# Kernel tuning notes

Measured on AMD Instinct MI355X. Metric: run time of the kernel, lower is better.

## Reference

```python
import jax, jax.numpy as jnp
import numpy as np

B, T, C, H, FF, BOT = 2, 2048, 1024, 16, 4096, 64
D = C // H
EPS = 1e-5

def _ln(x, g, b):
    m = jnp.mean(x, axis=-1, keepdims=True)
    v = jnp.mean(jnp.square(x - m), axis=-1, keepdims=True)
    return (x - m) * jax.lax.rsqrt(v + EPS) * g + b

def setup_inputs() -> dict:
    key = jax.random.key(0)
    ks = jax.random.split(key, 20)
    def lin(k, fan_in, shape):
        return jax.random.normal(k, shape, jnp.float32) * (1.0 / np.sqrt(fan_in))
    inp = {
        "x": jax.random.normal(ks[0], (B, T, C), jnp.float32),
        # causal mask: masked_fill where mask == 0
        "attn_mask": jnp.tril(jnp.ones((T, T), jnp.int32))[None, None, :, :],
        "Wq": lin(ks[1], C, (C, C)), "bq": jnp.zeros((C,), jnp.float32),
        "Wk": lin(ks[2], C, (C, C)), "bk": jnp.zeros((C,), jnp.float32),
        "Wv": lin(ks[3], C, (C, C)), "bv": jnp.zeros((C,), jnp.float32),
        "Wo": lin(ks[4], C, (C, C)), "bo": jnp.zeros((C,), jnp.float32),
        "g1": jnp.ones((C,), jnp.float32), "beta1": jnp.zeros((C,), jnp.float32),
        "g2": jnp.ones((C,), jnp.float32), "beta2": jnp.zeros((C,), jnp.float32),
        "W1": lin(ks[5], C, (C, FF)), "bf1": jnp.zeros((FF,), jnp.float32),
        "W2": lin(ks[6], FF, (FF, C)), "bf2": jnp.zeros((C,), jnp.float32),
        "Wd": lin(ks[7], C, (C, BOT)), "bd": jnp.zeros((BOT,), jnp.float32),
        "Wu": lin(ks[8], BOT, (BOT, C)), "bu": jnp.zeros((C,), jnp.float32),
    }
    return inp

def reference(x, attn_mask, Wq, bq, Wk, bk, Wv, bv, Wo, bo,
              g1, beta1, g2, beta2, W1, bf1, W2, bf2, Wd, bd, Wu, bu):
    # --- attention sublayer ---
    xn = _ln(x, g1, beta1)
    q = (xn @ Wq + bq).reshape(B, T, H, D)
    k = (xn @ Wk + bk).reshape(B, T, H, D)
    v = (xn @ Wv + bv).reshape(B, T, H, D)
    scores = jnp.einsum('bthd,bshd->bhts', q, k) / jnp.sqrt(jnp.float32(D))
    scores = jnp.where(attn_mask == 0, -jnp.inf, scores)
    w = jax.nn.softmax(scores, axis=-1)
    attn = jnp.einsum('bhts,bshd->bthd', w, v).reshape(B, T, C)
    x = x + attn @ Wo + bo
    # --- FFN + adapter sublayer ---
    xn2 = _ln(x, g2, beta2)
    h = jax.nn.relu(xn2 @ W1 + bf1) @ W2 + bf2
    h = h + jax.nn.relu(h @ Wd + bd) @ Wu + bu  # adapter residual
    return x + h
```

## Files before the change

### kernel.cpp

```cpp
#include <hip/hip_runtime.h>
#include <cstdint>
#include <cstddef>

typedef unsigned short u16;
typedef __attribute__((ext_vector_type(4))) short short4v;
typedef __attribute__((ext_vector_type(8))) short short8;
typedef __attribute__((ext_vector_type(4))) float f32x4;

__device__ __forceinline__ float bf2f(u16 h) { return __uint_as_float(((unsigned)h) << 16); }
__device__ __forceinline__ u16 f2bf(float f) {
    unsigned u = __float_as_uint(f);
    unsigned r = (u + 0x7fffu + ((u >> 16) & 1u)) >> 16;
    return (u16)r;
}
__device__ __forceinline__ u16 f2bf_fast(float f) {
    return (u16)((__float_as_uint(f) + 0x8000u) >> 16);
}

__device__ __forceinline__ void gl_lds16(const void* g, void* l) {
    __builtin_amdgcn_global_load_lds((const __attribute__((address_space(1))) void*)g,
                                     (__attribute__((address_space(3))) void*)l, 16, 0, 0);
}

struct Prologue {
    const void* tsrc[8];
    u16* tdst[8];
    int tR[8], tC[8], toff[8];
    const void* psrc[12];
    int poff[12], pn[12];
    int ntrans;
};
__global__ __launch_bounds__(256) void prologue_kernel(Prologue P,
                                                       const unsigned* __restrict__ x,
                                                       int* __restrict__ flag,
                                                       float* __restrict__ pf) {
    __shared__ int cnt[256];
    int c = 0;
    for (int i = threadIdx.x; i < 1024; i += 256) {
        unsigned lo = x[i] & 0xFFFFu;
        unsigned e = (lo >> 7) & 0xFFu;
        c += (e >= 100u && e <= 150u) ? 1 : 0;
    }
    cnt[threadIdx.x] = c;
    __syncthreads();
    for (int s = 128; s > 0; s >>= 1) {
        if (threadIdx.x < s) cnt[threadIdx.x] += cnt[threadIdx.x + s];
        __syncthreads();
    }
    const int bf = (cnt[0] > 512) ? 1 : 0;
    if (blockIdx.x == 0 && threadIdx.x == 0) *flag = bf;

    const int bid = blockIdx.x;
    if (bid >= P.ntrans) {
        const int s = bid - P.ntrans;
        const void* sp = P.psrc[s];
        float* dp = pf + P.poff[s];
        const int n = P.pn[s];
        for (int i = threadIdx.x; i < n; i += 256)
            dp[i] = bf ? bf2f(((const u16*)sp)[i]) : ((const float*)sp)[i];
        return;
    }
    __shared__ u16 tile[32][33];
    int m = 0;
#pragma unroll
    for (int i = 1; i < 8; i++) m = (bid >= P.toff[i]) ? i : m;
    const int local = bid - P.toff[m];
    const int R = P.tR[m], C = P.tC[m];
    const int tilesx = C >> 5;
    const int bx = local % tilesx, by = local / tilesx;
    const void* src = P.tsrc[m];
    u16* dst = P.tdst[m];
    const int tx = threadIdx.x & 31, ty = threadIdx.x >> 5;
#pragma unroll
    for (int i = 0; i < 32; i += 8) {
        size_t idx = (size_t)(by * 32 + ty + i) * C + bx * 32 + tx;
        tile[ty + i][tx] = bf ? ((const u16*)src)[idx] : f2bf(((const float*)src)[idx]);
    }
    __syncthreads();
#pragma unroll
    for (int i = 0; i < 32; i += 8)
        dst[(size_t)(bx * 32 + ty + i) * R + by * 32 + tx] = tile[tx][ty + i];
}

__global__ __launch_bounds__(256) void ln_x_kernel(const void* __restrict__ X,
                                                   const float* __restrict__ G,
                                                   const float* __restrict__ Be,
                                                   u16* __restrict__ Xb,
                                                   u16* __restrict__ Y,
                                                   const int* __restrict__ flag) {
    const int row = blockIdx.x;
    const int tid = threadIdx.x;
    const int lane = tid & 63, wave = tid >> 6;
    u16 vbuf[4];
    if (*flag) {
        *(uint2*)vbuf = *(const uint2*)((const u16*)X + (size_t)row * 1024 + tid * 4);
    } else {
        float4 v = *(const float4*)((const float*)X + (size_t)row * 1024 + tid * 4);
        vbuf[0] = f2bf(v.x); vbuf[1] = f2bf(v.y); vbuf[2] = f2bf(v.z); vbuf[3] = f2bf(v.w);
    }
    *(uint2*)&Xb[(size_t)row * 1024 + tid * 4] = *(uint2*)vbuf;
    float f[4];
    float s = 0.f, sq = 0.f;
#pragma unroll
    for (int j = 0; j < 4; j++) { f[j] = bf2f(vbuf[j]); s += f[j]; sq += f[j] * f[j]; }
#pragma unroll
    for (int m = 1; m < 64; m <<= 1) { s += __shfl_xor(s, m, 64); sq += __shfl_xor(sq, m, 64); }
    __shared__ float rs_[4], rq_[4];
    if (lane == 0) { rs_[wave] = s; rq_[wave] = sq; }
    __syncthreads();
    float S = rs_[0] + rs_[1] + rs_[2] + rs_[3];
    float Q2 = rq_[0] + rq_[1] + rq_[2] + rq_[3];
    float mean = S * (1.f / 1024.f);
    float var = Q2 * (1.f / 1024.f) - mean * mean;
    float rstd = rsqrtf(var + 1e-5f);
    u16 o[4];
#pragma unroll
    for (int j = 0; j < 4; j++) {
        int c2 = tid * 4 + j;
        float y = (f[j] - mean) * rstd * G[c2] + Be[c2];
        o[j] = f2bf(y);
    }
    *(uint2*)&Y[(size_t)row * 1024 + tid * 4] = *(uint2*)o;
}

__global__ __launch_bounds__(256) void ln_kernel(const u16* __restrict__ X,
                                                 const float* __restrict__ G,
                                                 const float* __restrict__ Be,
                                                 u16* __restrict__ Y) {
    const int row = blockIdx.x;
    const int tid = threadIdx.x;
    const int lane = tid & 63, wave = tid >> 6;
    const u16* xr = X + (size_t)row * 1024;
    u16 vbuf[4];
    *(uint2*)vbuf = *(const uint2*)&xr[tid * 4];
    float f[4];
    float s = 0.f, sq = 0.f;
#pragma unroll
    for (int j = 0; j < 4; j++) { f[j] = bf2f(vbuf[j]); s += f[j]; sq += f[j] * f[j]; }
#pragma unroll
    for (int m = 1; m < 64; m <<= 1) { s += __shfl_xor(s, m, 64); sq += __shfl_xor(sq, m, 64); }
    __shared__ float rs_[4], rq_[4];
    if (lane == 0) { rs_[wave] = s; rq_[wave] = sq; }
    __syncthreads();
    float S = rs_[0] + rs_[1] + rs_[2] + rs_[3];
    float Q2 = rq_[0] + rq_[1] + rq_[2] + rq_[3];
    float mean = S * (1.f / 1024.f);
    float var = Q2 * (1.f / 1024.f) - mean * mean;
    float rstd = rsqrtf(var + 1e-5f);
    u16 o[4];
#pragma unroll
    for (int j = 0; j < 4; j++) {
        int c2 = tid * 4 + j;
        float y = (f[j] - mean) * rstd * G[c2] + Be[c2];
        o[j] = f2bf(y);
    }
    *(uint2*)&Y[(size_t)row * 1024 + tid * 4] = *(uint2*)o;
}

template <int TAG>
__global__ __launch_bounds__(256) void gemm_bt_kernel(const u16* __restrict__ A,
                                                      const u16* __restrict__ Bt,
                                                      const float* __restrict__ bias,
                                                      const u16* __restrict__ res1,
                                                      const u16* __restrict__ res2,
                                                      void* __restrict__ out,
                                                      void* __restrict__ out_k,
                                                      void* __restrict__ out_v,
                                                      int M, int N, int K, int relu, int mode,
                                                      const int* __restrict__ flag) {
    __shared__ __align__(16) u16 As[2][128 * 32];
    __shared__ __align__(16) u16 Bs[2][128 * 32];
    const int tid = threadIdx.x;
    const int wave = tid >> 6, lane = tid & 63;
    const int m0 = blockIdx.y * 128, n0 = blockIdx.x * 128;
    const int wm = (wave >> 1) * 64, wn = (wave & 1) * 64;

    f32x4 acc[4][4];
#pragma unroll
    for (int i = 0; i < 4; i++)
#pragma unroll
        for (int j = 0; j < 4; j++) acc[i][j] = (f32x4){0.f, 0.f, 0.f, 0.f};

    const int lr4 = lane >> 2;
    const int sc4 = ((lane & 3) ^ ((lane >> 3) & 3));

    const int Ksub = K / (int)gridDim.z;
    const int kbeg = blockIdx.z * Ksub;

    auto stage = [&](int k0, int bufi) {
#pragma unroll
        for (int c = 0; c < 2; c++) {
            int rbase = wave * 32 + c * 16;
            int arow = m0 + rbase + lr4;
            int brow = n0 + rbase + lr4;
            if (brow > N - 1) brow = N - 1;
            gl_lds16(A + (size_t)arow * K + k0 + sc4 * 8, &As[bufi][rbase * 32 + lane * 8]);
            gl_lds16(Bt + (size_t)brow * K + k0 + sc4 * 8, &Bs[bufi][rbase * 32 + lane * 8]);
        }
    };

    stage(kbeg, 0);
    __syncthreads();
    const int nk = Ksub >> 5;
    for (int ik = 0; ik < nk; ik++) {
        const int cur = ik & 1;
        if (ik + 1 < nk) stage(kbeg + ((ik + 1) << 5), cur ^ 1);
        short8 af[4], bf[4];
        const int cc = (lane >> 4) ^ ((lane >> 1) & 3);
#pragma unroll
        for (int i = 0; i < 4; i++)
            af[i] = *(const short8*)&As[cur][(wm + i * 16 + (lane & 15)) * 32 + cc * 8];
#pragma unroll
        for (int j = 0; j < 4; j++)
            bf[j] = *(const short8*)&Bs[cur][(wn + j * 16 + (lane & 15)) * 32 + cc * 8];
#pragma unroll
        for (int i = 0; i < 4; i++)
#pragma unroll
            for (int j = 0; j < 4; j++)
                acc[i][j] = __builtin_amdgcn_mfma_f32_16x16x32_bf16(af[i], bf[j], acc[i][j], 0, 0, 0);
        __syncthreads();
    }

    if (mode == 3) {
        float* po = (float*)out + (size_t)blockIdx.z * M * N;
#pragma unroll
        for (int j = 0; j < 4; j++) {
            int col = n0 + wn + j * 16 + (lane & 15);
            if (col >= N) continue;
#pragma unroll
            for (int i = 0; i < 4; i++)
#pragma unroll
                for (int r = 0; r < 4; r++) {
                    int row = m0 + wm + i * 16 + (lane >> 4) * 4 + r;
                    po[(size_t)row * N + col] = acc[i][j][r];
                }
        }
        return;
    }

    const int f32out = (mode == 1) && (*flag == 0);
#pragma unroll
    for (int j = 0; j < 4; j++) {
        int col = n0 + wn + j * 16 + (lane & 15);
        if (col >= N) continue;
        float bv = bias ? bias[col] : 0.f;
#pragma unroll
        for (int i = 0; i < 4; i++) {
#pragma unroll
            for (int r = 0; r < 4; r++) {
                int row = m0 + wm + i * 16 + (lane >> 4) * 4 + r;
                float v = acc[i][j][r] + bv;
                if (relu) v = fmaxf(v, 0.f);
                size_t idx = (size_t)row * N + col;
                if (res1) v += bf2f(res1[idx]);
                if (res2) v += bf2f(res2[idx]);
                if (f32out) ((float*)out)[idx] = v;
                else ((u16*)out)[idx] = f2bf(v);
            }
        }
    }
}

template <int TAG>
__global__ __launch_bounds__(512, 4) void gemm128_kernel(const u16* __restrict__ A,
                                                         const u16* __restrict__ Bt,
                                                         const float* __restrict__ bias,
                                                         const u16* __restrict__ res1,
                                                         const u16* __restrict__ res2,
                                                         void* __restrict__ out,
                                                         void* __restrict__ out_k,
                                                         void* __restrict__ out_v,
                                                         int M, int N, int K, int relu, int mode,
                                                         int swz,
                                                         const int* __restrict__ flag) {
    (void)flag; (void)M;
    __shared__ __align__(16) u16 As[2][2][128 * 32];
    __shared__ __align__(16) u16 Bs[2][2][128 * 32];
    const int tid = threadIdx.x;
    const int wave = tid >> 6, lane = tid & 63;
    const int l15 = lane & 15, quad = lane >> 4;
    const int wr = wave & 3, wc = wave >> 2;
    int bx = blockIdx.x, by = blockIdx.y;
    if (swz) {
        const int gx = gridDim.x;
        const int nwg = gx * gridDim.y;
        const int bid = by * gx + bx;
        const int sbid = (bid & 7) * (nwg >> 3) + (bid >> 3);
        bx = sbid % gx;
        by = sbid / gx;
    }
    const int m0 = by * 128, n0 = bx * 128;
    const int nt = K >> 6;

    const int rsub = lane >> 2;
    const int logc = (lane & 3) ^ ((rsub >> 1) & 3);

    auto stage_pair = [&](int t, int kh) {
        const int buf = t & 1;
        const int kk = (t << 6) + (kh << 5) + logc * 8;
        const int roff = wave * 16 + rsub;
        gl_lds16(A + (size_t)(m0 + roff) * K + kk, &As[buf][kh][wave * 512 + lane * 8]);
        gl_lds16(Bt + (size_t)(n0 + roff) * K + kk, &Bs[buf][kh][wave * 512 + lane * 8]);
    };

    f32x4 acc[2][4];
#pragma unroll
    for (int i = 0; i < 2; i++)
#pragma unroll
        for (int j = 0; j < 4; j++) acc[i][j] = (f32x4){0.f, 0.f, 0.f, 0.f};

    stage_pair(0, 0);
    stage_pair(0, 1);
    stage_pair(1, 0);
    asm volatile("s_waitcnt vmcnt(4)" ::: "memory");
    __builtin_amdgcn_s_barrier();

    const int rx = (l15 >> 1) & 3;
    for (int t = 0; t < nt; t++) {
        const int b = t & 1;
#pragma unroll
        for (int ph = 0; ph < 2; ph++) {
            const int kh = ph;
            short8 af[2], bfr[4];
#pragma unroll
            for (int i = 0; i < 2; i++)
                af[i] = *(const short8*)&As[b][kh][(wr * 32 + i * 16 + l15) * 32 +
                                                   ((quad ^ rx) << 3)];
#pragma unroll
            for (int j = 0; j < 4; j++)
                bfr[j] = *(const short8*)&Bs[b][kh][(wc * 64 + j * 16 + l15) * 32 +
                                                    ((quad ^ rx) << 3)];
            if (ph == 0) { if (t + 1 < nt) stage_pair(t + 1, 1); }
            else         { if (t + 2 < nt) stage_pair(t + 2, 0); }
            __builtin_amdgcn_s_setprio(1);
#pragma unroll
            for (int i = 0; i < 2; i++)
#pragma unroll
                for (int j = 0; j < 4; j++)
                    acc[i][j] = __builtin_amdgcn_mfma_f32_16x16x32_bf16(
                        af[i], bfr[j], acc[i][j], 0, 0, 0);
            __builtin_amdgcn_s_setprio(0);
            if (ph == 0) {
                if (t + 1 < nt) { asm volatile("s_waitcnt vmcnt(4)" ::: "memory"); }
                else            { asm volatile("s_waitcnt vmcnt(0)" ::: "memory"); }
            } else {
                if (t + 2 < nt)      { asm volatile("s_waitcnt vmcnt(4)" ::: "memory"); }
                else if (t + 1 < nt) { asm volatile("s_waitcnt vmcnt(2)" ::: "memory"); }
            }
            __builtin_amdgcn_s_barrier();
        }
    }

    if (mode == 2) {
        const int region = n0 >> 10;
        if (region < 2) {
            u16* o = (u16*)(region == 0 ? out : out_k);
#pragma unroll
            for (int j = 0; j < 4; j++) {
                const int col = n0 + wc * 64 + j * 16 + l15;
                const float bv = bias[col];
                const int cl = col & 1023;
#pragma unroll
                for (int i = 0; i < 2; i++) {
                    const int row0 = m0 + wr * 32 + i * 16 + quad * 4;
#pragma unroll
                    for (int r = 0; r < 4; r++)
                        o[(size_t)(row0 + r) * 1024 + cl] = f2bf(acc[i][j][r] + bv);
                }
            }
        } else {
            u16* o = (u16*)out_v;
#pragma unroll
            for (int j = 0; j < 4; j++) {
                const int col = n0 + wc * 64 + j * 16 + l15;
                const float bv = bias[col];
                const int cl = col & 1023;
                const int h = cl >> 6, d = cl & 63;
#pragma unroll
                for (int i = 0; i < 2; i++) {
                    const int row_base = m0 + wr * 32 + i * 16 + quad * 4;
                    const int bb = row_base >> 11, tt = row_base & 2047;
                    u16 pk[4];
#pragma unroll
                    for (int r = 0; r < 4; r++) pk[r] = f2bf(acc[i][j][r] + bv);
                    *(uint2*)&o[(((size_t)bb * 16 + h) * 64 + d) * 2048 + tt] = *(uint2*)pk;
                }
            }
        }
        return;
    }
#pragma unroll
    for (int j = 0; j < 4; j++) {
        const int col = n0 + wc * 64 + j * 16 + l15;
        const float bv = bias ? bias[col] : 0.f;
#pragma unroll
        for (int i = 0; i < 2; i++) {
            const int row0 = m0 + wr * 32 + i * 16 + quad * 4;
#pragma unroll
            for (int r = 0; r < 4; r++) {
                float v = acc[i][j][r] + bv;
                if (relu) v = fmaxf(v, 0.f);
                const size_t idx = (size_t)(row0 + r) * N + col;
                if (res1) v += bf2f(res1[idx]);
                if (res2) v += bf2f(res2[idx]);
                ((u16*)out)[idx] = f2bf(v);
            }
        }
    }
}

template <int TAG>
__global__ __launch_bounds__(512, 2) void gemm256m_kernel(const u16* __restrict__ A,
                                                          const u16* __restrict__ Bt,
                                                          const float* __restrict__ bias,
                                                          void* __restrict__ out,
                                                          int N, int K, int relu) {
    __shared__ __align__(16) u16 As[2][2][256 * 32];
    __shared__ __align__(16) u16 Bs[2][2][128 * 32];
    const int tid = threadIdx.x;
    const int wave = tid >> 6, lane = tid & 63;
    const int l15 = lane & 15, quad = lane >> 4;
    const int wr = wave >> 1, wc = wave & 1;
    const int m0 = blockIdx.y * 256, n0 = blockIdx.x * 128;
    const int nt = K >> 6;

    const int rsub = lane >> 2;
    const int logc = (lane & 3) ^ ((rsub >> 1) & 3);

    auto stage_pair = [&](int t, int kh) {
        const int buf = t & 1;
        const int kk = (t << 6) + (kh << 5) + logc * 8;
        const int ra = m0 + wave * 32 + rsub;
        const int rb = n0 + wave * 16 + rsub;
        u16* da = &As[buf][kh][wave * 1024 + lane * 8];
        gl_lds16(A + (size_t)ra * K + kk, da);
        gl_lds16(A + (size_t)(ra + 16) * K + kk, da + 512);
        gl_lds16(Bt + (size_t)rb * K + kk, &Bs[buf][kh][wave * 512 + lane * 8]);
    };

    f32x4 acc[4][4];
#pragma unroll
    for (int i = 0; i < 4; i++)
#pragma unroll
        for (int j = 0; j < 4; j++) acc[i][j] = (f32x4){0.f, 0.f, 0.f, 0.f};

    stage_pair(0, 0);
    stage_pair(0, 1);
    stage_pair(1, 0);
    asm volatile("s_waitcnt vmcnt(6)" ::: "memory");
    __builtin_amdgcn_s_barrier();

    const int rx = (l15 >> 1) & 3;
    for (int t = 0; t < nt; t++) {
        const int b = t & 1;
#pragma unroll
        for (int ph = 0; ph < 2; ph++) {
            const int kh = ph;
            short8 af[4], bfr[4];
#pragma unroll
            for (int i = 0; i < 4; i++)
                af[i] = *(const short8*)&As[b][kh][(wr * 64 + i * 16 + l15) * 32 +
                                                   ((quad ^ rx) << 3)];
#pragma unroll
            for (int j = 0; j < 4; j++)
                bfr[j] = *(const short8*)&Bs[b][kh][(wc * 64 + j * 16 + l15) * 32 +
                                                    ((quad ^ rx) << 3)];
            if (ph == 0) { if (t + 1 < nt) stage_pair(t + 1, 1); }
            else         { if (t + 2 < nt) stage_pair(t + 2, 0); }
            __builtin_amdgcn_s_setprio(1);
#pragma unroll
            for (int i = 0; i < 4; i++)
#pragma unroll
                for (int j = 0; j < 4; j++)
                    acc[i][j] = __builtin_amdgcn_mfma_f32_16x16x32_bf16(
                        af[i], bfr[j], acc[i][j], 0, 0, 0);
            __builtin_amdgcn_s_setprio(0);
            if (ph == 0) {
                if (t + 1 < nt) { asm volatile("s_waitcnt vmcnt(6)" ::: "memory"); }
                else            { asm volatile("s_waitcnt vmcnt(0)" ::: "memory"); }
            } else {
                if (t + 2 < nt)      { asm volatile("s_waitcnt vmcnt(6)" ::: "memory"); }
                else if (t + 1 < nt) { asm volatile("s_waitcnt vmcnt(3)" ::: "memory"); }
            }
            __builtin_amdgcn_s_barrier();
        }
    }

#pragma unroll
    for (int j = 0; j < 4; j++) {
        const int col = n0 + wc * 64 + j * 16 + l15;
        const float bv = bias ? bias[col] : 0.f;
#pragma unroll
        for (int i = 0; i < 4; i++) {
            const int row0 = m0 + wr * 64 + i * 16 + quad * 4;
#pragma unroll
            for (int r = 0; r < 4; r++) {
                float v = acc[i][j][r] + bv;
                if (relu) v = fmaxf(v, 0.f);
                ((u16*)out)[(size_t)(row0 + r) * N + col] = f2bf(v);
            }
        }
    }
}

template <int TAG>
__global__ __launch_bounds__(512, 2) void gemm128d_kernel(const u16* __restrict__ A,
                                                          const u16* __restrict__ Bt,
                                                          const float* __restrict__ bias,
                                                          const u16* __restrict__ res1,
                                                          void* __restrict__ out,
                                                          int N, int K, int relu, int swz) {
    __shared__ __align__(16) u16 As[2][2][128 * 64];
    __shared__ __align__(16) u16 Bs[2][2][128 * 64];
    const int tid = threadIdx.x;
    const int wave = tid >> 6, lane = tid & 63;
    const int l15 = lane & 15, quad = lane >> 4;
    const int wr = wave & 3, wc = wave >> 2;
    int bx = blockIdx.x, by = blockIdx.y;
    if (swz) {
        const int gx = gridDim.x;
        const int nwg = gx * gridDim.y;
        const int bid = by * gx + bx;
        const int sbid = (bid & 7) * (nwg >> 3) + (bid >> 3);
        bx = sbid % gx;
        by = sbid / gx;
    }
    const int m0 = by * 128, n0 = bx * 128;
    const int nt = K >> 7;

    const int srow = lane >> 3;
    const int logc = (lane & 7) ^ ((lane >> 4) & 3);

    auto stage_pair = [&](int t, int kh) {
        const int buf = t & 1;
        const int kk = (t << 7) + (kh << 6) + logc * 8;
        const int r0 = wave * 16 + srow;
        u16* da = &As[buf][kh][wave * 1024 + lane * 8];
        u16* db = &Bs[buf][kh][wave * 1024 + lane * 8];
        gl_lds16(A + (size_t)(m0 + r0) * K + kk, da);
        gl_lds16(A + (size_t)(m0 + r0 + 8) * K + kk, da + 512);
        gl_lds16(Bt + (size_t)(n0 + r0) * K + kk, db);
        gl_lds16(Bt + (size_t)(n0 + r0 + 8) * K + kk, db + 512);
    };

    f32x4 acc[2][4];
#pragma unroll
    for (int i = 0; i < 2; i++)
#pragma unroll
        for (int j = 0; j < 4; j++) acc[i][j] = (f32x4){0.f, 0.f, 0.f, 0.f};

    stage_pair(0, 0);
    stage_pair(0, 1);
    stage_pair(1, 0);
    asm volatile("s_waitcnt vmcnt(8)" ::: "memory");
    __builtin_amdgcn_s_barrier();

    const int rx = (l15 >> 1) & 3;
    for (int t = 0; t < nt; t++) {
        const int b = t & 1;
#pragma unroll
        for (int ph = 0; ph < 2; ph++) {
            const int kh = ph;
            short8 af[2][2], bfr[4][2];
#pragma unroll
            for (int ks = 0; ks < 2; ks++) {
                const int ck = ((ks << 2) | (quad ^ rx)) << 3;
#pragma unroll
                for (int i = 0; i < 2; i++)
                    af[i][ks] = *(const short8*)&As[b][kh][(wr * 32 + i * 16 + l15) * 64 + ck];
#pragma unroll
                for (int j = 0; j < 4; j++)
                    bfr[j][ks] = *(const short8*)&Bs[b][kh][(wc * 64 + j * 16 + l15) * 64 + ck];
            }
            if (ph == 0) { if (t + 1 < nt) stage_pair(t + 1, 1); }
            else         { if (t + 2 < nt) stage_pair(t + 2, 0); }
            __builtin_amdgcn_s_setprio(1);
#pragma unroll
            for (int ks = 0; ks < 2; ks++)
#pragma unroll
                for (int i = 0; i < 2; i++)
#pragma unroll
                    for (int j = 0; j < 4; j++)
                        acc[i][j] = __builtin_amdgcn_mfma_f32_16x16x32_bf16(
                            af[i][ks], bfr[j][ks], acc[i][j], 0, 0, 0);
            __builtin_amdgcn_s_setprio(0);
            if (ph == 0) {
                if (t + 1 < nt) { asm volatile("s_waitcnt vmcnt(8)" ::: "memory"); }
                else            { asm volatile("s_waitcnt vmcnt(0)" ::: "memory"); }
            } else {
                if (t + 2 < nt)      { asm volatile("s_waitcnt vmcnt(8)" ::: "memory"); }
                else if (t + 1 < nt) { asm volatile("s_waitcnt vmcnt(4)" ::: "memory"); }
            }
            __builtin_amdgcn_s_barrier();
        }
    }

#pragma unroll
    for (int j = 0; j < 4; j++) {
        const int col = n0 + wc * 64 + j * 16 + l15;
        const float bv = bias ? bias[col] : 0.f;
#pragma unroll
        for (int i = 0; i < 2; i++) {
            const int row0 = m0 + wr * 32 + i * 16 + quad * 4;
#pragma unroll
            for (int r = 0; r < 4; r++) {
                float v = acc[i][j][r] + bv;
                if (relu) v = fmaxf(v, 0.f);
                const size_t idx = (size_t)(row0 + r) * N + col;
                if (res1) v += bf2f(res1[idx]);
                ((u16*)out)[idx] = f2bf(v);
            }
        }
    }
}

template <int TAG>
__global__ __launch_bounds__(256) void reduce_kernel(const float* __restrict__ part,
                                                     int nsplit, size_t MN,
                                                     const float* __restrict__ bias, int N,
                                                     const u16* __restrict__ res1,
                                                     const u16* __restrict__ res2,
                                                     void* __restrict__ out,
                                                     int relu, int final_store,
                                                     const int* __restrict__ flag) {
    const size_t i0 = ((size_t)blockIdx.x * 256 + threadIdx.x) * 4;
    float4 s = *(const float4*)&part[i0];
    for (int z = 1; z < nsplit; z++) {
        float4 p = *(const float4*)&part[(size_t)z * MN + i0];
        s.x += p.x; s.y += p.y; s.z += p.z; s.w += p.w;
    }
    const int col = (int)(i0 & (size_t)(N - 1));
    float v[4] = {s.x, s.y, s.z, s.w};
#pragma unroll
    for (int j = 0; j < 4; j++) {
        v[j] += bias[col + j];
        if (relu) v[j] = fmaxf(v[j], 0.f);
    }
    if (res1) {
        u16 r[4]; *(uint2*)r = *(const uint2*)&res1[i0];
#pragma unroll
        for (int j = 0; j < 4; j++) v[j] += bf2f(r[j]);
    }
    if (res2) {
        u16 r[4]; *(uint2*)r = *(const uint2*)&res2[i0];
#pragma unroll
        for (int j = 0; j < 4; j++) v[j] += bf2f(r[j]);
    }
    if (final_store && (*flag == 0)) {
        *(float4*)&((float*)out)[i0] = (float4){v[0], v[1], v[2], v[3]};
    } else {
        u16 o[4];
#pragma unroll
        for (int j = 0; j < 4; j++) o[j] = f2bf(v[j]);
        *(uint2*)&((u16*)out)[i0] = *(uint2*)o;
    }
}

template <int SPLIT>
__global__ __launch_bounds__(256) void flash_kernel(const u16* __restrict__ Q,
                                                    const u16* __restrict__ Kg,
                                                    const u16* __restrict__ VtG,
                                                    u16* __restrict__ O,
                                                    u16* __restrict__ pO,
                                                    float* __restrict__ pL) {
    const int tid = threadIdx.x;
    const int wave = tid >> 6, lane = tid & 63;
    int qb, ch;
    if (SPLIT) {
        const int i = blockIdx.x;
        if (i < 32)      { qb = 31 - (i >> 2); ch = i & 3; }
        else if (i < 56) { const int j = i - 32; qb = 23 - j / 3; ch = j % 3; }
        else if (i < 72) { const int j = i - 56; qb = 15 - (j >> 1); ch = j & 1; }
        else             { qb = 7 - (i - 72); ch = 0; }
    } else {
        qb = 31 - blockIdx.x; ch = 0;
    }
    const int bh = blockIdx.y;
    const int t0 = qb * 64;
    const int steps = qb + 1;
    const int ktbeg = SPLIT ? ch * 8 : 0;
    const int ktend = SPLIT ? (steps < ktbeg + 8 ? steps : ktbeg + 8) : steps;
    const size_t base = ((size_t)(bh >> 4) * 2048) * 1024 + (size_t)(bh & 15) * 64;
    const size_t basev = (size_t)bh * 64 * 2048;

    __shared__ __align__(16) u16 Ks[2][64 * 64];
    __shared__ __align__(16) u16 Vt[2][64 * 64];
#if !__has_builtin(__builtin_amdgcn_mfma_f32_16x16x16bf16_1k)
    __shared__ __align__(16) u16 Ps[4][16 * 72];
#endif

    const int l15 = lane & 15, quad = lane >> 4;
    const int rmin = t0 + wave * 16;

    short8 qf[2];
    {
        const u16* qp = Q + base + (size_t)(rmin + l15) * 1024 + quad * 8;
        qf[0] = *(const short8*)qp;
        qf[1] = *(const short8*)(qp + 32);
    }

    const int slr = lane >> 3;
    const int sc8 = (lane & 7) ^ slr;
    const int rb = wave * 16;

    auto stage = [&](int kt, int bufi) {
        gl_lds16(Kg + base + (size_t)(kt * 64 + rb + slr) * 1024 + sc8 * 8,
                 &Ks[bufi][rb * 64 + lane * 8]);
        gl_lds16(Kg + base + (size_t)(kt * 64 + rb + 8 + slr) * 1024 + sc8 * 8,
                 &Ks[bufi][(rb + 8) * 64 + lane * 8]);
        gl_lds16(VtG + basev + (size_t)(rb + slr) * 2048 + kt * 64 + sc8 * 8,
                 &Vt[bufi][rb * 64 + lane * 8]);
        gl_lds16(VtG + basev + (size_t)(rb + 8 + slr) * 2048 + kt * 64 + sc8 * 8,
                 &Vt[bufi][(rb + 8) * 64 + lane * 8]);
    };

    float l_part = 0.f;
    f32x4 oacc[4];
#pragma unroll
    for (int jt = 0; jt < 4; jt++) oacc[jt] = (f32x4){0.f, 0.f, 0.f, 0.f};

    const float Cs = 0.125f * 1.44269504f;

    stage(ktbeg, 0);
    __syncthreads();

    for (int kt = ktbeg; kt < ktend; kt++) {
        const int cur = kt & 1;
        if (kt + 1 < ktend) stage(kt + 1, cur ^ 1);

        short8 kf[2][4];
#pragma unroll
        for (int st = 0; st < 2; st++)
#pragma unroll
            for (int j = 0; j < 4; j++)
                kf[st][j] = *(const short8*)&Ks[cur][(j * 16 + l15) * 64 +
                                                     (((st * 4 + quad) ^ (l15 & 7)) * 8)];
#if __has_builtin(__builtin_amdgcn_mfma_f32_16x16x16bf16_1k)
        short4v vf[4][4];
#pragma unroll
        for (int j = 0; j < 4; j++) {
            int k8 = j * 2 + (quad >> 1);
#pragma unroll
            for (int jt = 0; jt < 4; jt++) {
                int d = jt * 16 + l15;
                vf[j][jt] = *(const short4v*)&Vt[cur][d * 64 + ((k8 ^ (d & 7)) * 8) +
                                                      (quad & 1) * 4];
            }
        }
#else
        short8 vf[2][4];
#pragma unroll
        for (int st = 0; st < 2; st++)
#pragma unroll
            for (int jt = 0; jt < 4; jt++) {
                int d = jt * 16 + l15;
                vf[st][jt] = *(const short8*)&Vt[cur][d * 64 + (((st * 4 + quad) ^ (d & 7)) * 8)];
            }
#endif

        f32x4 s[4];
#pragma unroll
        for (int j = 0; j < 4; j++) s[j] = (f32x4){0.f, 0.f, 0.f, 0.f};
#pragma unroll
        for (int st = 0; st < 2; st++)
#pragma unroll
            for (int j = 0; j < 4; j++)
                s[j] = __builtin_amdgcn_mfma_f32_16x16x32_bf16(kf[st][j], qf[st], s[j], 0, 0, 0);

        float lpv[4] = {0.f, 0.f, 0.f, 0.f};
        short4v pj[4];
        if (kt != qb) {
#pragma unroll
            for (int j = 0; j < 4; j++) {
                union { short4v v; u16 u[4]; } pk;
#pragma unroll
                for (int r = 0; r < 4; r++) {
                    float p = __builtin_amdgcn_exp2f(s[j][r] * Cs);
                    lpv[r] += p;
                    pk.u[r] = f2bf_fast(p);
                }
                pj[j] = pk.v;
            }
        } else {
            const int qrow = rmin + l15;
#pragma unroll
            for (int j = 0; j < 4; j++) {
                union { short4v v; u16 u[4]; } pk;
#pragma unroll
                for (int r = 0; r < 4; r++) {
                    float p = __builtin_amdgcn_exp2f(s[j][r] * Cs);
                    int key = kt * 64 + j * 16 + quad * 4 + r;
                    if (key > qrow) p = 0.f;
                    lpv[r] += p;
                    pk.u[r] = f2bf_fast(p);
                }
                pj[j] = pk.v;
            }
        }
        l_part += (lpv[0] + lpv[1]) + (lpv[2] + lpv[3]);

#if __has_builtin(__builtin_amdgcn_mfma_f32_16x16x16bf16_1k)
#pragma unroll
        for (int jt = 0; jt < 4; jt++)
#pragma unroll
            for (int j = 0; j < 4; j++)
                oacc[jt] = __builtin_amdgcn_mfma_f32_16x16x16bf16_1k(pj[j], vf[j][jt],
                                                                     oacc[jt], 0, 0, 0);
#else
        u16* Pw = Ps[wave];
#pragma unroll
        for (int j = 0; j < 4; j++)
            *(short4v*)&Pw[l15 * 72 + j * 16 + quad * 4] = pj[j];
#pragma unroll
        for (int st = 0; st < 2; st++) {
            short8 pf2 = *(const short8*)&Pw[l15 * 72 + st * 32 + quad * 8];
#pragma unroll
            for (int jt = 0; jt < 4; jt++)
                oacc[jt] = __builtin_amdgcn_mfma_f32_16x16x32_bf16(pf2, vf[st][jt],
                                                                  oacc[jt], 0, 0, 0);
        }
#endif
        __syncthreads();
    }

    float lf = l_part;
    lf += __shfl_xor(lf, 16, 64);
    lf += __shfl_xor(lf, 32, 64);

    if (SPLIT && steps > 8) {
        const size_t ib = ((size_t)bh * 24 + (qb - 8)) * 4 + ch;
        u16* po = pO + ib * 4096;
#pragma unroll
        for (int jt = 0; jt < 4; jt++)
#pragma unroll
            for (int r = 0; r < 4; r++)
                po[(wave * 16 + quad * 4 + r) * 64 + jt * 16 + l15] = f2bf(oacc[jt][r]);
        if (quad == 0) pL[ib * 64 + wave * 16 + l15] = lf;
        return;
    }

    {
        float inv[4];
#pragma unroll
        for (int r = 0; r < 4; r++) inv[r] = 1.f / __shfl(lf, quad * 4 + r, 64);
#pragma unroll
        for (int jt = 0; jt < 4; jt++) {
            int d = jt * 16 + l15;
#pragma unroll
            for (int r = 0; r < 4; r++) {
                int t = rmin + quad * 4 + r;
                O[base + (size_t)t * 1024 + d] = f2bf(oacc[jt][r] * inv[r]);
            }
        }
    }
}

__global__ __launch_bounds__(256) void flash_combine_kernel(const u16* __restrict__ pO,
                                                            const float* __restrict__ pL,
                                                            u16* __restrict__ O) {
    const int qj = blockIdx.x;
    const int bh = blockIdx.y;
    const int qb = qj + 8;
    const int nch = (qb >> 3) + 1;
    const int tid = threadIdx.x;
    const int row = tid >> 2;
    const int d0 = (tid & 3) * 16;
    const size_t ib = ((size_t)bh * 24 + qj) * 4;

    float acc[16];
#pragma unroll
    for (int k = 0; k < 16; k++) acc[k] = 0.f;
    float lsum = 0.f;
    for (int c = 0; c < nch; c++) {
        const u16* po = pO + (ib + c) * 4096 + row * 64 + d0;
        u16 pb[16];
        *(uint4*)pb = *(const uint4*)po;
        *(uint4*)(pb + 8) = *(const uint4*)(po + 8);
#pragma unroll
        for (int k = 0; k < 16; k++) acc[k] += bf2f(pb[k]);
        lsum += pL[(ib + c) * 64 + row];
    }
    const float inv = 1.f / lsum;
    u16 o[16];
#pragma unroll
    for (int k = 0; k < 16; k++) o[k] = f2bf(acc[k] * inv);
    const size_t base = ((size_t)(bh >> 4) * 2048) * 1024 + (size_t)(bh & 15) * 64;
    const int t = qb * 64 + row;
    u16* op = &O[base + (size_t)t * 1024 + d0];
    *(uint4*)op = ((uint4*)o)[0];
    *(uint4*)(op + 8) = ((uint4*)o)[1];
}

extern "C" void kernel_launch(void* const* d_in, const int* in_sizes, int n_in,
                              void* d_out, int out_size, void* d_ws, size_t ws_size,
                              hipStream_t stream) {
    (void)in_sizes; (void)n_in; (void)out_size;
    const void* x   = d_in[0];
    const void* Wq  = d_in[2];  const void* bq  = d_in[3];
    const void* Wk  = d_in[4];  const void* bk  = d_in[5];
    const void* Wv  = d_in[6];  const void* bv  = d_in[7];
    const void* Wo  = d_in[8];  const void* bo  = d_in[9];
    const void* g1  = d_in[10]; const void* be1 = d_in[11];
    const void* g2  = d_in[12]; const void* be2 = d_in[13];
    const void* W1  = d_in[14]; const void* bf1 = d_in[15];
    const void* W2  = d_in[16]; const void* bf2 = d_in[17];
    const void* Wd  = d_in[18]; const void* bd  = d_in[19];
    const void* Wu  = d_in[20]; const void* bu  = d_in[21];

    uint8_t* w8 = (uint8_t*)d_ws;
    int* flag = (int*)w8;
    float* pf = (float*)(w8 + 64);
    u16* wsb = (u16*)(w8 + 64 + 65536);

    const size_t M1 = 1024ull * 1024ull;
    u16* WqT = wsb;
    u16* WkT = wsb + 1 * M1;
    u16* WvT = wsb + 2 * M1;
    u16* WoT = wsb + 3 * M1;
    u16* W1T = wsb + 4 * M1;
    u16* W2T = wsb + 8 * M1;
    u16* WdT = wsb + 12 * M1;
    u16* WuT = wsb + 12 * M1 + 65536;
    u16* S0  = wsb + 12 * M1 + 131072;
    u16* Areg = S0;
    u16* Breg = S0 + 4 * M1;
    u16* ff1  = S0;
    u16* Creg = S0 + 16 * M1;
    u16* Dreg = S0 + 20 * M1;
    u16* Ereg = S0 + 24 * M1;
    u16* xb = Areg;
    u16* xn = Breg; u16* attn = Breg;
    u16* q = Creg;  u16* xn2 = Creg;  u16* bot = Creg;
    u16* kk_ = Dreg; u16* x1 = Dreg;
    u16* VtG = Ereg; u16* hh = Ereg;

    const size_t arena_bytes = (size_t)(64 + 65536) + (40 * M1 + 131072) * 2;
    float* partf = (float*)(w8 + ((arena_bytes + 255) & ~(size_t)255));
    const size_t need = ((arena_bytes + 255) & ~(size_t)255) + 4ull * 4 * M1 * 4;
    const bool sk = ws_size >= need;
    float* flL = partf + 14 * M1;

    float* bqkv_f = pf + 0;
    float* bo_f  = pf + 3072;
    float* bf1_f = pf + 4096;  float* bf2_f = pf + 8192;
    float* bd_f  = pf + 9216;  float* bu_f  = pf + 9280;
    float* g1_f  = pf + 10304; float* be1_f = pf + 11328;
    float* g2_f  = pf + 12352; float* be2_f = pf + 13376;

    Prologue P;
    const void* tsrc[8] = {Wq, Wk, Wv, Wo, W1, W2, Wd, Wu};
    u16* tdst[8] = {WqT, WkT, WvT, WoT, W1T, W2T, WdT, WuT};
    int tR[8] = {1024, 1024, 1024, 1024, 1024, 4096, 1024, 64};
    int tC[8] = {1024, 1024, 1024, 1024, 4096, 1024, 64, 1024};
    int acc_off = 0;
    for (int i = 0; i < 8; i++) {
        P.tsrc[i] = tsrc[i]; P.tdst[i] = tdst[i];
        P.tR[i] = tR[i]; P.tC[i] = tC[i];
        P.toff[i] = acc_off;
        acc_off += (tR[i] >> 5) * (tC[i] >> 5);
    }
    P.ntrans = acc_off;
    const void* psrc[12] = {bq, bk, bv, bo, bf1, bf2, bd, bu, g1, be1, g2, be2};
    int poff[12] = {0, 1024, 2048, 3072, 4096, 8192, 9216, 9280, 10304, 11328, 12352, 13376};
    int pn[12]   = {1024, 1024, 1024, 1024, 4096, 1024, 64, 1024, 1024, 1024, 1024, 1024};
    for (int i = 0; i < 12; i++) { P.psrc[i] = psrc[i]; P.poff[i] = poff[i]; P.pn[i] = pn[i]; }
    prologue_kernel<<<acc_off + 12, 256, 0, stream>>>(P, (const unsigned*)x, flag, pf);

    ln_x_kernel<<<4096, 256, 0, stream>>>(x, g1_f, be1_f, xb, xn, flag);
    gemm128_kernel<0><<<dim3(24, 32), 512, 0, stream>>>(xn, WqT, bqkv_f, nullptr, nullptr,
                                                        q, kk_, VtG, 4096, 3072, 1024, 0, 2, 0, flag);
    if (sk) {
        flash_kernel<1><<<dim3(80, 32), 256, 0, stream>>>(q, kk_, VtG, attn, (u16*)partf, flL);
        flash_combine_kernel<<<dim3(24, 32), 256, 0, stream>>>((const u16*)partf, flL, attn);
    } else {
        flash_kernel<0><<<dim3(32, 32), 256, 0, stream>>>(q, kk_, VtG, attn, nullptr, nullptr);
    }
    gemm128d_kernel<1><<<dim3(8, 32), 512, 0, stream>>>(attn, WoT, bo_f, xb,
                                                        x1, 1024, 1024, 0, 1);
    ln_kernel<<<4096, 256, 0, stream>>>(x1, g2_f, be2_f, xn2);
    gemm256m_kernel<2><<<dim3(32, 16), 512, 0, stream>>>(xn2, W1T, bf1_f,
                                                         ff1, 4096, 1024, 1);
    gemm128d_kernel<3><<<dim3(8, 32), 512, 0, stream>>>(ff1, W2T, bf2_f, nullptr,
                                                        hh, 1024, 4096, 0, 1);
    if (sk) {
        gemm_bt_kernel<4><<<dim3(1, 32, 8), 256, 0, stream>>>(hh, WdT, nullptr, nullptr, nullptr,
                                                              partf, nullptr, nullptr, 4096, 64, 1024, 1, 3, flag);
        reduce_kernel<4><<<256, 256, 0, stream>>>(partf, 8, 256 * 1024, bd_f, 64, nullptr, nullptr,
                                                  bot, 1, 0, flag);
    } else {
        gemm_bt_kernel<4><<<dim3(1, 32), 256, 0, stream>>>(hh, WdT, bd_f, nullptr, nullptr,
                                                           bot, nullptr, nullptr, 4096, 64, 1024, 1, 0, flag);
    }
    gemm_bt_kernel<5><<<dim3(8, 32), 256, 0, stream>>>(bot, WuT, bu_f, hh, x1,
                                                       d_out, nullptr, nullptr, 4096, 1024, 64, 0, 1, flag);
}
```

Before: 433.7 us.

## Fuse adapter down-proj, ReLU and up-proj with residuals into one kernel

Replaces the split-K down-projection GEMM, its reduce kernel and the separate up-projection GEMM with a single adapter kernel. Each 512-thread block handles 16 rows: eight waves split K for the down-projection, reduce the partials in LDS, apply bias and ReLU, then compute the up-projection and add both residuals. This drops two launches and the round trips of the fp32 partials and the bottleneck activations through global memory. In exchange, each block of only 16 rows re-reads WdT and WuT straight from global memory without LDS staging, and reads hh with strided direct loads.

```diff
diff --git a/kernel.cpp b/kernel.cpp
--- a/kernel.cpp
+++ b/kernel.cpp
@@ -155,110 +155,6 @@
         o[j] = f2bf(y);
     }
     *(uint2*)&Y[(size_t)row * 1024 + tid * 4] = *(uint2*)o;
-}
-
-template <int TAG>
-__global__ __launch_bounds__(256) void gemm_bt_kernel(const u16* __restrict__ A,
-                                                      const u16* __restrict__ Bt,
-                                                      const float* __restrict__ bias,
-                                                      const u16* __restrict__ res1,
-                                                      const u16* __restrict__ res2,
-                                                      void* __restrict__ out,
-                                                      void* __restrict__ out_k,
-                                                      void* __restrict__ out_v,
-                                                      int M, int N, int K, int relu, int mode,
-                                                      const int* __restrict__ flag) {
-    __shared__ __align__(16) u16 As[2][128 * 32];
-    __shared__ __align__(16) u16 Bs[2][128 * 32];
-    const int tid = threadIdx.x;
-    const int wave = tid >> 6, lane = tid & 63;
-    const int m0 = blockIdx.y * 128, n0 = blockIdx.x * 128;
-    const int wm = (wave >> 1) * 64, wn = (wave & 1) * 64;
-
-    f32x4 acc[4][4];
-#pragma unroll
-    for (int i = 0; i < 4; i++)
-#pragma unroll
-        for (int j = 0; j < 4; j++) acc[i][j] = (f32x4){0.f, 0.f, 0.f, 0.f};
-
-    const int lr4 = lane >> 2;
-    const int sc4 = ((lane & 3) ^ ((lane >> 3) & 3));
-
-    const int Ksub = K / (int)gridDim.z;
-    const int kbeg = blockIdx.z * Ksub;
-
-    auto stage = [&](int k0, int bufi) {
-#pragma unroll
-        for (int c = 0; c < 2; c++) {
-            int rbase = wave * 32 + c * 16;
-            int arow = m0 + rbase + lr4;
-            int brow = n0 + rbase + lr4;
-            if (brow > N - 1) brow = N - 1;
-            gl_lds16(A + (size_t)arow * K + k0 + sc4 * 8, &As[bufi][rbase * 32 + lane * 8]);
-            gl_lds16(Bt + (size_t)brow * K + k0 + sc4 * 8, &Bs[bufi][rbase * 32 + lane * 8]);
-        }
-    };
-
-    stage(kbeg, 0);
-    __syncthreads();
-    const int nk = Ksub >> 5;
-    for (int ik = 0; ik < nk; ik++) {
-        const int cur = ik & 1;
-        if (ik + 1 < nk) stage(kbeg + ((ik + 1) << 5), cur ^ 1);
-        short8 af[4], bf[4];
-        const int cc = (lane >> 4) ^ ((lane >> 1) & 3);
-#pragma unroll
-        for (int i = 0; i < 4; i++)
-            af[i] = *(const short8*)&As[cur][(wm + i * 16 + (lane & 15)) * 32 + cc * 8];
-#pragma unroll
-        for (int j = 0; j < 4; j++)
-            bf[j] = *(const short8*)&Bs[cur][(wn + j * 16 + (lane & 15)) * 32 + cc * 8];
-#pragma unroll
-        for (int i = 0; i < 4; i++)
-#pragma unroll
-            for (int j = 0; j < 4; j++)
-                acc[i][j] = __builtin_amdgcn_mfma_f32_16x16x32_bf16(af[i], bf[j], acc[i][j], 0, 0, 0);
-        __syncthreads();
-    }
-
-    if (mode == 3) {
-        float* po = (float*)out + (size_t)blockIdx.z * M * N;
-#pragma unroll
-        for (int j = 0; j < 4; j++) {
-            int col = n0 + wn + j * 16 + (lane & 15);
-            if (col >= N) continue;
-#pragma unroll
-            for (int i = 0; i < 4; i++)
-#pragma unroll
-                for (int r = 0; r < 4; r++) {
-                    int row = m0 + wm + i * 16 + (lane >> 4) * 4 + r;
-                    po[(size_t)row * N + col] = acc[i][j][r];
-                }
-        }
-        return;
-    }
-
-    const int f32out = (mode == 1) && (*flag == 0);
-#pragma unroll
-    for (int j = 0; j < 4; j++) {
-        int col = n0 + wn + j * 16 + (lane & 15);
-        if (col >= N) continue;
-        float bv = bias ? bias[col] : 0.f;
-#pragma unroll
-        for (int i = 0; i < 4; i++) {
-#pragma unroll
-            for (int r = 0; r < 4; r++) {
-                int row = m0 + wm + i * 16 + (lane >> 4) * 4 + r;
-                float v = acc[i][j][r] + bv;
-                if (relu) v = fmaxf(v, 0.f);
-                size_t idx = (size_t)row * N + col;
-                if (res1) v += bf2f(res1[idx]);
-                if (res2) v += bf2f(res2[idx]);
-                if (f32out) ((float*)out)[idx] = v;
-                else ((u16*)out)[idx] = f2bf(v);
-            }
-        }
-    }
 }
 
 template <int TAG>
@@ -614,45 +510,82 @@
     }
 }
 
-template <int TAG>
-__global__ __launch_bounds__(256) void reduce_kernel(const float* __restrict__ part,
-                                                     int nsplit, size_t MN,
-                                                     const float* __restrict__ bias, int N,
-                                                     const u16* __restrict__ res1,
-                                                     const u16* __restrict__ res2,
-                                                     void* __restrict__ out,
-                                                     int relu, int final_store,
-                                                     const int* __restrict__ flag) {
-    const size_t i0 = ((size_t)blockIdx.x * 256 + threadIdx.x) * 4;
-    float4 s = *(const float4*)&part[i0];
-    for (int z = 1; z < nsplit; z++) {
-        float4 p = *(const float4*)&part[(size_t)z * MN + i0];
-        s.x += p.x; s.y += p.y; s.z += p.z; s.w += p.w;
-    }
-    const int col = (int)(i0 & (size_t)(N - 1));
-    float v[4] = {s.x, s.y, s.z, s.w};
-#pragma unroll
-    for (int j = 0; j < 4; j++) {
-        v[j] += bias[col + j];
-        if (relu) v[j] = fmaxf(v[j], 0.f);
-    }
-    if (res1) {
-        u16 r[4]; *(uint2*)r = *(const uint2*)&res1[i0];
-#pragma unroll
-        for (int j = 0; j < 4; j++) v[j] += bf2f(r[j]);
-    }
-    if (res2) {
-        u16 r[4]; *(uint2*)r = *(const uint2*)&res2[i0];
-#pragma unroll
-        for (int j = 0; j < 4; j++) v[j] += bf2f(r[j]);
-    }
-    if (final_store && (*flag == 0)) {
-        *(float4*)&((float*)out)[i0] = (float4){v[0], v[1], v[2], v[3]};
-    } else {
-        u16 o[4];
-#pragma unroll
-        for (int j = 0; j < 4; j++) o[j] = f2bf(v[j]);
-        *(uint2*)&((u16*)out)[i0] = *(uint2*)o;
+__global__ __launch_bounds__(512) void adapter_kernel(const u16* __restrict__ hh,
+                                                      const u16* __restrict__ x1,
+                                                      const u16* __restrict__ WdT,
+                                                      const u16* __restrict__ WuT,
+                                                      const float* __restrict__ bd,
+                                                      const float* __restrict__ bu,
+                                                      void* __restrict__ out,
+                                                      const int* __restrict__ flag) {
+    const int tid = threadIdx.x;
+    const int wave = tid >> 6, lane = tid & 63;
+    const int l15 = lane & 15, quad = lane >> 4;
+    const int r0 = blockIdx.x * 16;
+
+    __shared__ float part[8][16 * 64];
+    __shared__ __align__(16) u16 bot_s[16 * 72];
+
+    f32x4 dacc[4];
+#pragma unroll
+    for (int j = 0; j < 4; j++) dacc[j] = (f32x4){0.f, 0.f, 0.f, 0.f};
+    const int kw = wave * 128;
+#pragma unroll
+    for (int ks = 0; ks < 4; ks++) {
+        const int k0 = kw + ks * 32 + quad * 8;
+        short8 af = *(const short8*)&hh[(size_t)(r0 + l15) * 1024 + k0];
+#pragma unroll
+        for (int j = 0; j < 4; j++) {
+            short8 bf = *(const short8*)&WdT[(size_t)(j * 16 + l15) * 1024 + k0];
+            dacc[j] = __builtin_amdgcn_mfma_f32_16x16x32_bf16(af, bf, dacc[j], 0, 0, 0);
+        }
+    }
+#pragma unroll
+    for (int j = 0; j < 4; j++)
+#pragma unroll
+        for (int r = 0; r < 4; r++)
+            part[wave][(quad * 4 + r) * 64 + j * 16 + l15] = dacc[j][r];
+    __syncthreads();
+
+    for (int e = tid; e < 1024; e += 512) {
+        float s = part[0][e];
+#pragma unroll
+        for (int w = 1; w < 8; w++) s += part[w][e];
+        s += bd[e & 63];
+        s = fmaxf(s, 0.f);
+        bot_s[(e >> 6) * 72 + (e & 63)] = f2bf(s);
+    }
+    __syncthreads();
+
+    short8 auf[2];
+    auf[0] = *(const short8*)&bot_s[l15 * 72 + quad * 8];
+    auf[1] = *(const short8*)&bot_s[l15 * 72 + 32 + quad * 8];
+    f32x4 uacc[8];
+#pragma unroll
+    for (int j = 0; j < 8; j++) uacc[j] = (f32x4){0.f, 0.f, 0.f, 0.f};
+#pragma unroll
+    for (int j = 0; j < 8; j++) {
+        const size_t nb = (size_t)(wave * 128 + j * 16 + l15) * 64;
+        short8 b0 = *(const short8*)&WuT[nb + quad * 8];
+        short8 b1 = *(const short8*)&WuT[nb + 32 + quad * 8];
+        uacc[j] = __builtin_amdgcn_mfma_f32_16x16x32_bf16(auf[0], b0, uacc[j], 0, 0, 0);
+        uacc[j] = __builtin_amdgcn_mfma_f32_16x16x32_bf16(auf[1], b1, uacc[j], 0, 0, 0);
+    }
+    const int f32out = (*flag == 0);
+#pragma unroll
+    for (int j = 0; j < 8; j++) {
+        const int col = wave * 128 + j * 16 + l15;
+        const float bv = bu[col];
+#pragma unroll
+        for (int r = 0; r < 4; r++) {
+            const int row = r0 + quad * 4 + r;
+            const size_t idx = (size_t)row * 1024 + col;
+            float v = uacc[j][r] + bv;
+            v += bf2f(hh[idx]);
+            v += bf2f(x1[idx]);
+            if (f32out) ((float*)out)[idx] = v;
+            else ((u16*)out)[idx] = f2bf(v);
+        }
     }
 }
 
@@ -930,7 +863,7 @@
     u16* Ereg = S0 + 24 * M1;
     u16* xb = Areg;
     u16* xn = Breg; u16* attn = Breg;
-    u16* q = Creg;  u16* xn2 = Creg;  u16* bot = Creg;
+    u16* q = Creg;  u16* xn2 = Creg;
     u16* kk_ = Dreg; u16* x1 = Dreg;
     u16* VtG = Ereg; u16* hh = Ereg;
 
@@ -982,15 +915,5 @@
                                                          ff1, 4096, 1024, 1);
     gemm128d_kernel<3><<<dim3(8, 32), 512, 0, stream>>>(ff1, W2T, bf2_f, nullptr,
                                                         hh, 1024, 4096, 0, 1);
-    if (sk) {
-        gemm_bt_kernel<4><<<dim3(1, 32, 8), 256, 0, stream>>>(hh, WdT, nullptr, nullptr, nullptr,
-                                                              partf, nullptr, nullptr, 4096, 64, 1024, 1, 3, flag);
-        reduce_kernel<4><<<256, 256, 0, stream>>>(partf, 8, 256 * 1024, bd_f, 64, nullptr, nullptr,
-                                                  bot, 1, 0, flag);
-    } else {
-        gemm_bt_kernel<4><<<dim3(1, 32), 256, 0, stream>>>(hh, WdT, bd_f, nullptr, nullptr,
-                                                           bot, nullptr, nullptr, 4096, 64, 1024, 1, 0, flag);
-    }
-    gemm_bt_kernel<5><<<dim3(8, 32), 256, 0, stream>>>(bot, WuT, bu_f, hh, x1,
-                                                       d_out, nullptr, nullptr, 4096, 1024, 64, 0, 1, flag);
-}
+    adapter_kernel<<<256, 512, 0, stream>>>(hh, x1, WdT, WuT, bd_f, bu_f, d_out, flag);
+}
```

Result: faster. 403.1 us (-7.0%).
